# Kernel optimization log

Measured on AMD Instinct MI355X. Metric: run time of the kernel, lower is better.

The kernel has to match this reference:

```python
import jax, jax.numpy as jnp
import numpy as np
from jax import lax

# Model dims (match init_kwargs config)
HID = 2048      # hidden_size
NH = 64         # num_heads
P = 64          # head_dim
N = 128         # ssm_state_size
G = 1           # n_groups
CS = 256        # chunk_size
K = 4           # conv kernel
D_INNER = NH * P                  # 4096
CONV_DIM = D_INNER + 2 * G * N    # 4352
PROJ = D_INNER + CONV_DIM + NH    # 8512
EPS = 1e-5
BATCH, SEQ = 2, 2048


def setup_inputs() -> dict:
    key = jax.random.key(0)
    ks = jax.random.split(key, 8)
    hidden_states = jax.random.normal(ks[0], (BATCH, SEQ, HID), dtype=jnp.float32)
    W_in = jax.random.normal(ks[1], (PROJ, HID), dtype=jnp.float32) * 0.02
    conv_w = jax.random.normal(ks[2], (CONV_DIM, 1, K), dtype=jnp.float32) * 0.2
    conv_b = jax.random.normal(ks[3], (CONV_DIM,), dtype=jnp.float32) * 0.02
    # dt_bias initialized like inv-softplus of dt in [1e-3, 1e-1]
    dt = jnp.exp(jax.random.uniform(ks[4], (NH,)) * (np.log(0.1) - np.log(0.001)) + np.log(0.001))
    dt_bias = (dt + jnp.log(-jnp.expm1(-dt))).astype(jnp.float32)
    A_log = jnp.log(jnp.arange(1, NH + 1, dtype=jnp.float32))
    D_param = jnp.ones((NH,), dtype=jnp.float32)
    norm_w = jnp.ones((D_INNER,), dtype=jnp.float32)
    W_out = jax.random.normal(ks[5], (HID, D_INNER), dtype=jnp.float32) * 0.02
    return {"hidden_states": hidden_states, "W_in": W_in, "conv_w": conv_w,
            "conv_b": conv_b, "dt_bias": dt_bias, "A_log": A_log,
            "D_param": D_param, "norm_w": norm_w, "W_out": W_out}


def _segsum(x):
    # x: (..., c) -> (..., c, c); seg[i, j] = sum_{j < k <= i} x_k (diag 0), -inf above diag
    T = x.shape[-1]
    xc = jnp.cumsum(x, axis=-1)
    seg = xc[..., :, None] - xc[..., None, :]
    mask = jnp.tril(jnp.ones((T, T), dtype=bool))
    return jnp.where(mask, seg, -jnp.inf)


def _mamba2_forward(hidden_states, W_in, conv_w, conv_b, dt_bias, A_log, D_param, norm_w, W_out):
    B_, L_ = hidden_states.shape[:2]
    proj = hidden_states @ W_in.T                           # (b, l, PROJ)
    z = proj[..., :D_INNER]                                 # gate
    xBC = proj[..., D_INNER:D_INNER + CONV_DIM]
    dt = proj[..., D_INNER + CONV_DIM:]                     # (b, l, NH)

    # depthwise causal conv1d + silu
    xc = lax.conv_general_dilated(
        jnp.transpose(xBC, (0, 2, 1)), conv_w,
        window_strides=(1,), padding=[(K - 1, 0)],
        feature_group_count=CONV_DIM)                        # (b, CONV_DIM, l)
    xc = xc + conv_b[None, :, None]
    xBC = jax.nn.silu(jnp.transpose(xc, (0, 2, 1)))          # (b, l, CONV_DIM)

    x = xBC[..., :D_INNER].reshape(B_, L_, NH, P)
    Bm = xBC[..., D_INNER:D_INNER + G * N].reshape(B_, L_, G, N)
    Cm = xBC[..., D_INNER + G * N:].reshape(B_, L_, G, N)

    dt = jax.nn.softplus(dt + dt_bias)                       # (b, l, NH)
    A = -jnp.exp(A_log)                                      # (NH,)

    Bh = jnp.repeat(Bm, NH // G, axis=2)                     # (b, l, h, n)
    Ch = jnp.repeat(Cm, NH // G, axis=2)

    # ---- chunked SSD scan ----
    nc = L_ // CS
    x_dt = (x * dt[..., None]).reshape(B_, nc, CS, NH, P)    # (b, c, s, h, p)
    B_c = Bh.reshape(B_, nc, CS, NH, N)
    C_c = Ch.reshape(B_, nc, CS, NH, N)
    dA = jnp.transpose((dt * A).reshape(B_, nc, CS, NH), (0, 3, 1, 2))  # (b, h, c, s)
    A_cum = jnp.cumsum(dA, axis=-1)                          # (b, h, c, s)

    Lmat = jnp.exp(_segsum(dA))                              # (b, h, c, s, s)
    Y_diag = jnp.einsum('bclhn,bcshn,bhcls,bcshp->bclhp', C_c, B_c, Lmat, x_dt)

    decay_states = jnp.exp(A_cum[..., -1:] - A_cum)          # (b, h, c, s)
    states = jnp.einsum('bclhn,bhcl,bclhp->bchpn', B_c, decay_states, x_dt)

    da_last = A_cum[..., -1]                                 # (b, h, c)

    def step(prev, inp):
        s_k, d_k = inp                                       # (b,h,p,n), (b,h)
        new = prev * jnp.exp(d_k)[..., None, None] + s_k
        return new, prev

    _, prev_states = lax.scan(step, jnp.zeros((B_, NH, P, N), dtype=x.dtype),
                              (jnp.transpose(states, (1, 0, 2, 3, 4)),
                               jnp.transpose(da_last, (2, 0, 1))))
    prev_states = jnp.transpose(prev_states, (1, 2, 0, 3, 4))  # (b, h, c, p, n)

    Y_off = jnp.einsum('bclhn,bhcpn,bhcl->bclhp', C_c, prev_states, jnp.exp(A_cum))

    y = (Y_diag + Y_off).reshape(B_, L_, NH, P) + D_param[None, None, :, None] * x
    y = y.reshape(B_, L_, D_INNER)

    # gated grouped RMSNorm (norm_before_gate=False): norm(y * silu(z)) * w
    g = y * jax.nn.silu(z)
    gs = D_INNER // G
    gr = g.reshape(B_, L_, G, gs)
    var = jnp.mean(gr * gr, axis=-1, keepdims=True)
    gn = (gr * lax.rsqrt(var + EPS)).reshape(B_, L_, D_INNER) * norm_w

    return gn @ W_out.T                                      # (b, l, HID)


def reference(hidden_states, W_in, conv_w, conv_b, dt_bias, A_log, D_param, norm_w, W_out):
    return _mamba2_forward(hidden_states, W_in, conv_w, conv_b, dt_bias, A_log, D_param, norm_w, W_out)
```

## Files before the change

kernel.cpp:

```cpp
#include <hip/hip_runtime.h>

#define SEQLEN 2048
#define NHEADS 64
#define PDIM 64
#define NSTATE 128
#define CSIZE 256
#define NCHUNK 8
#define DINNER 4096
#define CONVD 4352
#define PROJD 8512

using s8v = __attribute__((ext_vector_type(8))) short;
using f4v = __attribute__((ext_vector_type(4))) float;
using bf8v = __attribute__((ext_vector_type(8))) __bf16;

__device__ __forceinline__ short f2bf(float x) {
  union { float f; unsigned u; } t; t.f = x;
  unsigned r = t.u + 0x7FFFu + ((t.u >> 16) & 1u);
  return (short)(r >> 16);
}
__device__ __forceinline__ float bf2f(short s) {
  union { unsigned u; float f; } t;
  t.u = ((unsigned)(unsigned short)s) << 16;
  return t.f;
}

__device__ __forceinline__ f4v mfma_bf16(s8v a, s8v b, f4v c) {
  return __builtin_amdgcn_mfma_f32_16x16x32_bf16(
      __builtin_bit_cast(bf8v, a), __builtin_bit_cast(bf8v, b), c, 0, 0, 0);
}

__device__ __forceinline__ void gll16(const void* g, void* l) {
  __builtin_amdgcn_global_load_lds(
      (const __attribute__((address_space(1))) unsigned*)g,
      (__attribute__((address_space(3))) unsigned*)l, 16, 0, 0);
}

__global__ __launch_bounds__(256) void cast_bf16_kernel(
    const float* __restrict__ in, short* __restrict__ out, int n4) {
  int i = blockIdx.x * 256 + threadIdx.x;
  if (i < n4) {
    float4 v = ((const float4*)in)[i];
    short4 o;
    o.x = f2bf(v.x); o.y = f2bf(v.y); o.z = f2bf(v.z); o.w = f2bf(v.w);
    ((short4*)out)[i] = o;
  }
}


#define G1_STAGE_A(dst, h, kt) do {                                          \
    _Pragma("unroll")                                                        \
    for (int it_ = 0; it_ < 2; ++it_) {                                      \
      int ci_ = it_ * 512 + tid;                                             \
      int r_ = ci_ >> 3;                                                     \
      int g_ = ((ci_ & 7) ^ (r_ & 7)) << 3;                                  \
      gll16(&A[(size_t)(tm0 + (h) * 128 + r_) * 2048 + (kt) * 64 + g_],      \
            &(dst)[(h) * 8192 + ci_ * 8]);                                   \
    }                                                                        \
  } while (0)

#define G1_STAGE_B(dst, h, kt) do {                                          \
    _Pragma("unroll")                                                        \
    for (int it_ = 0; it_ < 2; ++it_) {                                      \
      int ci_ = it_ * 512 + tid;                                             \
      int r_ = ci_ >> 3;                                                     \
      int g_ = ((ci_ & 7) ^ (r_ & 7)) << 3;                                  \
      int br_ = tn0 + (h) * 128 + r_;                                        \
      if (br_ > 8511) br_ = 8511;       \
      gll16(&B[(size_t)br_ * 2048 + (kt) * 64 + g_],                         \
            &(dst)[(h) * 8192 + ci_ * 8]);                                   \
    }                                                                        \
  } while (0)

#define RD_A(m, ks) \
  (*(const s8v*)&Ad[(wm + (m) * 16 + lr) * 64 + (((ks) * 4 + q) ^ sw7) * 8])
#define RD_B(n, ks) \
  (*(const s8v*)&Bd[(wn + (n) * 16 + lr) * 64 + (((ks) * 4 + q) ^ sw7) * 8])

#define G1_PHASE(m0, STAGE_STMT) do {                                        \
    s8v a00 = RD_A(m0, 0), a01 = RD_A(m0, 1);                                \
    s8v a10 = RD_A((m0) + 1, 0), a11 = RD_A((m0) + 1, 1);                    \
    STAGE_STMT;                                                              \
    __builtin_amdgcn_s_barrier();                                            \
    asm volatile("s_waitcnt lgkmcnt(0)" ::: "memory");                       \
    __builtin_amdgcn_s_setprio(1);                                           \
    _Pragma("unroll") for (int n = 0; n < 4; ++n)                            \
      acc[m0][n] = mfma_bf16(a00, bk0[n], acc[m0][n]);                       \
    _Pragma("unroll") for (int n = 0; n < 4; ++n)                            \
      acc[m0][n] = mfma_bf16(a01, bk1[n], acc[m0][n]);                       \
    _Pragma("unroll") for (int n = 0; n < 4; ++n)                            \
      acc[(m0) + 1][n] = mfma_bf16(a10, bk0[n], acc[(m0) + 1][n]);           \
    _Pragma("unroll") for (int n = 0; n < 4; ++n)                            \
      acc[(m0) + 1][n] = mfma_bf16(a11, bk1[n], acc[(m0) + 1][n]);           \
    __builtin_amdgcn_s_setprio(0);                                           \
    __builtin_amdgcn_s_barrier();                                            \
  } while (0)

__global__ __launch_bounds__(512, 2) void gemm1_256(
    const short* __restrict__ A, const short* __restrict__ B,
    short* __restrict__ z, short* __restrict__ xbc, float* __restrict__ dtb) {
  const int NT = 32;
  const int bid = blockIdx.x;
  const int sid = (bid & 7) * 68 + (bid >> 3);
  const int panel = sid / 136, rem = sid % 136;
  const int bx = rem >> 2, by = panel * 4 + (rem & 3);
  const int tm0 = by * 256, tn0 = bx * 256;
  __shared__ alignas(16) short lds[65536];
  const int tid = threadIdx.x;
  const int lane = tid & 63, wid = tid >> 6;
  const int wm = (wid >> 2) * 128, wn = (wid & 3) * 64;
  const int lr = lane & 15, q = lane >> 4;
  const int sw7 = lr & 7;

  f4v acc[8][4];
#pragma unroll
  for (int m = 0; m < 8; ++m)
#pragma unroll
    for (int n = 0; n < 4; ++n)
#pragma unroll
      for (int r = 0; r < 4; ++r) acc[m][n][r] = 0.f;

  {
    short* A0 = lds;
    short* B0 = lds + 16384;
    short* B1 = lds + 49152;
    G1_STAGE_A(A0, 0, 0); G1_STAGE_A(A0, 1, 0);
    G1_STAGE_B(B0, 0, 0); G1_STAGE_B(B0, 1, 0);
    G1_STAGE_B(B1, 0, 1); G1_STAGE_B(B1, 1, 1);
  }

  for (int t = 0; t < NT; ++t) {
    short* Ad = lds + ((t & 1) << 15);
    short* Bd = Ad + 16384;
    short* An = lds + (((t + 1) & 1) << 15);
    s8v bk0[4], bk1[4];
    if (t + 1 < NT) {
      G1_STAGE_A(An, 0, t + 1);
      asm volatile("s_waitcnt vmcnt(6)" ::: "memory");
    } else {
      asm volatile("s_waitcnt vmcnt(0)" ::: "memory");
    }
    __builtin_amdgcn_s_barrier();
#pragma unroll
    for (int n = 0; n < 4; ++n) { bk0[n] = RD_B(n, 0); bk1[n] = RD_B(n, 1); }
    {
      s8v a00 = RD_A(0, 0), a01 = RD_A(0, 1);
      s8v a10 = RD_A(1, 0), a11 = RD_A(1, 1);
      __builtin_amdgcn_s_setprio(1);
#pragma unroll
      for (int n = 0; n < 4; ++n) acc[0][n] = mfma_bf16(a00, bk0[n], acc[0][n]);
#pragma unroll
      for (int n = 0; n < 4; ++n) acc[0][n] = mfma_bf16(a01, bk1[n], acc[0][n]);
#pragma unroll
      for (int n = 0; n < 4; ++n) acc[1][n] = mfma_bf16(a10, bk0[n], acc[1][n]);
#pragma unroll
      for (int n = 0; n < 4; ++n) acc[1][n] = mfma_bf16(a11, bk1[n], acc[1][n]);
      __builtin_amdgcn_s_setprio(0);
    }
    __builtin_amdgcn_s_barrier();
    G1_PHASE(2, if (t + 1 < NT) G1_STAGE_A(An, 1, t + 1));
    G1_PHASE(4, if (t + 2 < NT) G1_STAGE_B(Bd, 0, t + 2));
    G1_PHASE(6, if (t + 2 < NT) G1_STAGE_B(Bd, 1, t + 2));
  }

  if (bx == 33) {
    if (wn == 0) {
#pragma unroll
      for (int m = 0; m < 8; ++m)
#pragma unroll
        for (int n = 0; n < 4; ++n) {
          int col = n * 16 + lr;
#pragma unroll
          for (int r = 0; r < 4; ++r) {
            int row = tm0 + wm + m * 16 + q * 4 + r;
            dtb[(size_t)row * NHEADS + col] = acc[m][n][r];
          }
        }
    }
    return;
  }
  short* outp; int stride, colbase;
  if (bx < 16) { outp = z;   stride = DINNER; colbase = tn0; }
  else         { outp = xbc; stride = CONVD;  colbase = tn0 - DINNER; }
  short* Cs = lds;
  for (int h = 0; h < 2; ++h) {
    __syncthreads();
    if ((wid >> 2) == h) {
#pragma unroll
      for (int m = 0; m < 8; ++m)
#pragma unroll
        for (int n = 0; n < 4; ++n)
#pragma unroll
          for (int r = 0; r < 4; ++r)
            Cs[(m * 16 + q * 4 + r) * 264 + wn + n * 16 + lr] =
                f2bf(acc[m][n][r]);
    }
    __syncthreads();
#pragma unroll
    for (int itr = 0; itr < 8; ++itr) {
      int idx = itr * 512 + tid;
      int r = idx >> 5, c8 = (idx & 31) * 8;
      s8v v = *(const s8v*)&Cs[r * 264 + c8];
      *(s8v*)&outp[(size_t)(tm0 + h * 128 + r) * stride + colbase + c8] = v;
    }
  }
}

__global__ __launch_bounds__(256, 4) void gemm_nt_bf16(
    const short* __restrict__ A, const short* __restrict__ B,
    float* __restrict__ C, int M, int N, int K) {
  const int nbx = N >> 7;
  const int bid0 = blockIdx.x;
  const int bid = (bid0 & 7) * (gridDim.x >> 3) + (bid0 >> 3);
  const int panel = bid / (nbx * 4), rem = bid % (nbx * 4);
  const int bx = rem >> 2, by = panel * 4 + (rem & 3);
  const int tn0 = bx * 128, tm0 = by * 128;
  __shared__ alignas(16) short As[128 * 32];
  __shared__ alignas(16) short Bs[128 * 32];
  const int tid = threadIdx.x;
  const int lane = tid & 63, wid = tid >> 6;
  const int wm = (wid >> 1) * 64, wn = (wid & 1) * 64;
  const int lr = lane & 15, q = lane >> 4;
  const int fA = (lr & 3) ^ ((lr >> 2) & 3);
  const int qs = (q ^ fA) * 8;
  f4v acc[4][4];
  for (int i = 0; i < 4; i++)
    for (int j = 0; j < 4; j++)
      for (int r = 0; r < 4; r++) acc[i][j][r] = 0.f;

  for (int k0 = 0; k0 < K; k0 += 32) {
    __syncthreads();
    for (int it = 0; it < 2; it++) {
      int ci = it * 256 + tid;
      int row = ci >> 2;
      int cg = ((ci & 3) ^ (row & 3) ^ ((row >> 2) & 3)) << 3;
      gll16(&A[(size_t)(tm0 + row) * K + k0 + cg], &As[ci * 8]);
      gll16(&B[(size_t)(tn0 + row) * K + k0 + cg], &Bs[ci * 8]);
    }
    __syncthreads();
    s8v af[4], bfr[4];
    for (int i = 0; i < 4; i++) af[i]  = *(const s8v*)&As[(wm + i * 16 + lr) * 32 + qs];
    for (int j = 0; j < 4; j++) bfr[j] = *(const s8v*)&Bs[(wn + j * 16 + lr) * 32 + qs];
    for (int i = 0; i < 4; i++)
      for (int j = 0; j < 4; j++)
        acc[i][j] = mfma_bf16(af[i], bfr[j], acc[i][j]);
  }
  for (int i = 0; i < 4; i++)
    for (int j = 0; j < 4; j++) {
      int r0 = tm0 + wm + i * 16 + q * 4;
      int c0 = tn0 + wn + j * 16 + lr;
      for (int r = 0; r < 4; r++)
        C[(size_t)(r0 + r) * N + c0] = acc[i][j][r];
    }
}

__global__ __launch_bounds__(256) void conv_silu_kernel(
    const short* __restrict__ xbc, const float* __restrict__ conv_w,
    const float* __restrict__ conv_b, short* __restrict__ xBCc) {
  int cc = blockIdx.x * 256 + threadIdx.x;
  int bl = blockIdx.y;
  int b = bl >> 11, l = bl & 2047;
  float4 wv = *(const float4*)&conv_w[cc * 4];
  float wk[4] = {wv.x, wv.y, wv.z, wv.w};
  float acc = conv_b[cc];
  const short* pbase = xbc + (size_t)(b * SEQLEN) * CONVD + cc;
#pragma unroll
  for (int k = 0; k < 4; k++) {
    int ls = l - 3 + k;
    if (ls >= 0) acc += bf2f(pbase[(size_t)ls * CONVD]) * wk[k];
  }
  float sv = acc / (1.f + expf(-acc));
  xBCc[(size_t)bl * CONVD + cc] = f2bf(sv);
}

__global__ __launch_bounds__(256) void dt_kernel(
    float* __restrict__ dtb, const float* __restrict__ dt_bias) {
  int idx = blockIdx.x * 256 + threadIdx.x;
  int hh = idx & 63;
  float v = dtb[idx] + dt_bias[hh];
  dtb[idx] = (v > 20.f) ? v : log1pf(expf(v));
}

__global__ __launch_bounds__(256) void ssd_states_kernel(
    const short* __restrict__ xBCc, const float* __restrict__ dtp,
    const float* __restrict__ A_log, short* __restrict__ states,
    float* __restrict__ da_last) {
  const int blk = blockIdx.x;
  const int h = blk & 63, cc = (blk >> 6) & 7, b = blk >> 9;
  const int tid = threadIdx.x;
  __shared__ float dt_s[CSIZE], Acum[CSIZE], w_s[CSIZE];
  __shared__ float xw[64][64];
  __shared__ float Bt[64][NSTATE];
  const size_t row0 = (size_t)(b * SEQLEN + cc * CSIZE);
  dt_s[tid] = dtp[(row0 + tid) * NHEADS + h];
  __syncthreads();
  if (tid == 0) {
    float Aval = -expf(A_log[h]);
    float s = 0.f;
    for (int i = 0; i < CSIZE; i++) { s += dt_s[i]; Acum[i] = s * Aval; }
    da_last[(size_t)(b * NHEADS + h) * NCHUNK + cc] = Acum[CSIZE - 1];
  }
  __syncthreads();
  float total = Acum[CSIZE - 1];
  w_s[tid] = dt_s[tid] * expf(total - Acum[tid]);
  float acc[4][8];
  for (int a = 0; a < 4; a++) for (int j = 0; j < 8; j++) acc[a][j] = 0.f;
  const int pi = (tid & 15) * 4, ni = (tid >> 4) * 8;
  for (int lt = 0; lt < 4; lt++) {
    __syncthreads();
    for (int i = 0; i < 4; i++) {
      int idx = tid + i * 256;
      int r = idx >> 4, c4 = (idx & 15) << 2;
      short4 v = *(const short4*)&xBCc[(row0 + lt * 64 + r) * CONVD + h * PDIM + c4];
      float wl = w_s[lt * 64 + r];
      xw[r][c4 + 0] = bf2f(v.x) * wl;
      xw[r][c4 + 1] = bf2f(v.y) * wl;
      xw[r][c4 + 2] = bf2f(v.z) * wl;
      xw[r][c4 + 3] = bf2f(v.w) * wl;
    }
    for (int i = 0; i < 8; i++) {
      int idx = tid + i * 256;
      int r = idx >> 5, c4 = (idx & 31) << 2;
      short4 v = *(const short4*)&xBCc[(row0 + lt * 64 + r) * CONVD + DINNER + c4];
      Bt[r][c4 + 0] = bf2f(v.x);
      Bt[r][c4 + 1] = bf2f(v.y);
      Bt[r][c4 + 2] = bf2f(v.z);
      Bt[r][c4 + 3] = bf2f(v.w);
    }
    __syncthreads();
    for (int l = 0; l < 64; l++) {
      float4 xv = *(const float4*)&xw[l][pi];
      float4 b0 = *(const float4*)&Bt[l][ni];
      float4 b1 = *(const float4*)&Bt[l][ni + 4];
      float xa[4] = {xv.x, xv.y, xv.z, xv.w};
      float bb[8] = {b0.x, b0.y, b0.z, b0.w, b1.x, b1.y, b1.z, b1.w};
      for (int a = 0; a < 4; a++)
        for (int j = 0; j < 8; j++)
          acc[a][j] += xa[a] * bb[j];
    }
  }
  const size_t sbase = (((size_t)b * NCHUNK + cc) * NHEADS + h) * (PDIM * NSTATE);
  for (int a = 0; a < 4; a++) {
    short o[8];
    for (int j = 0; j < 8; j++) o[j] = f2bf(acc[a][j]);
    *(s8v*)&states[sbase + (size_t)(pi + a) * NSTATE + ni] = *(const s8v*)o;
  }
}

__global__ __launch_bounds__(256) void scan_kernel(
    short* __restrict__ states, const float* __restrict__ da_last) {
  const int bh = blockIdx.x >> 2, sl = blockIdx.x & 3;
  const int b = bh >> 6, h = bh & 63;
  const int tid = threadIdx.x;
  float prev[8];
  for (int i = 0; i < 8; i++) prev[i] = 0.f;
  for (int c = 0; c < NCHUNK; c++) {
    const size_t base = (((size_t)b * NCHUNK + c) * NHEADS + h) * (PDIM * NSTATE)
                      + sl * 2048;
    const float d = expf(da_last[(size_t)bh * NCHUNK + c]);
    for (int i = 0; i < 8; i++) {
      size_t e = base + tid + i * 256;
      float s = bf2f(states[e]);
      states[e] = f2bf(prev[i]);
      prev[i] = prev[i] * d + s;
    }
  }
}

__global__ __launch_bounds__(256) void ssd_y_kernel(
    const short* __restrict__ xBCc, const float* __restrict__ dtp,
    const float* __restrict__ A_log, const float* __restrict__ D_param,
    const short* __restrict__ prevs, short* __restrict__ y) {
  const int blk = blockIdx.x;
  const int h = blk & 63, cc = (blk >> 6) & 7, b = blk >> 9;
  const int tid = threadIdx.x;
  const int lane = tid & 63, w = tid >> 6;
  const int lr = lane & 15, q = lane >> 4;
  __shared__ float dt_s[CSIZE];
  __shared__ float Acum[CSIZE];
  __shared__ short C_s[64][136];
  __shared__ short BP_s[64][136];
  __shared__ short xdtT[64][72];
  __shared__ short Mt[64][72];
  const size_t row0 = (size_t)(b * SEQLEN + cc * CSIZE);
  dt_s[tid] = dtp[(row0 + tid) * NHEADS + h];
  __syncthreads();
  if (tid == 0) {
    float Aval = -expf(A_log[h]);
    float s = 0.f;
    for (int i = 0; i < CSIZE; i++) { s += dt_s[i]; Acum[i] = s * Aval; }
  }
  const float Dh = D_param[h];
  const size_t prevbase = (((size_t)b * NCHUNK + cc) * NHEADS + h) * (PDIM * NSTATE);
  const int wl0 = w * 16;

  for (int lt = 0; lt < 4; lt++) {
    __syncthreads();
    for (int i = 0; i < 4; i++) {
      int idx = tid + i * 256;
      int r = idx >> 4, c8 = (idx & 15) << 3;
      *(s8v*)&C_s[r][c8] =
          *(const s8v*)&xBCc[(row0 + lt * 64 + r) * CONVD + DINNER + NSTATE + c8];
      *(s8v*)&BP_s[r][c8] = *(const s8v*)&prevs[prevbase + (size_t)r * NSTATE + c8];
    }
    __syncthreads();
    f4v acc[4];
    for (int j = 0; j < 4; j++) for (int r = 0; r < 4; r++) acc[j][r] = 0.f;
    for (int ks = 0; ks < 4; ks++) {
      s8v a = *(const s8v*)&C_s[wl0 + lr][ks * 32 + q * 8];
      for (int j = 0; j < 4; j++) {
        s8v bb = *(const s8v*)&BP_s[j * 16 + lr][ks * 32 + q * 8];
        acc[j] = mfma_bf16(a, bb, acc[j]);
      }
    }
    for (int r = 0; r < 4; r++) {
      float e = __expf(Acum[lt * 64 + wl0 + q * 4 + r]);
      for (int j = 0; j < 4; j++) acc[j][r] *= e;
    }
    for (int st = 0; st <= lt; st++) {
      __syncthreads();
      for (int i = 0; i < 4; i++) {
        int idx = tid + i * 256;
        int r = idx >> 4, c8 = (idx & 15) << 3;
        *(s8v*)&BP_s[r][c8] =
            *(const s8v*)&xBCc[(row0 + st * 64 + r) * CONVD + DINNER + c8];
      }
      for (int i = 0; i < 4; i++) {
        int idx = tid + i * 256;
        int r = idx >> 4, c4 = (idx & 15) << 2;
        float dtv = dt_s[st * 64 + r];
        short4 v = *(const short4*)&xBCc[(row0 + st * 64 + r) * CONVD + h * PDIM + c4];
        xdtT[c4 + 0][r] = f2bf(bf2f(v.x) * dtv);
        xdtT[c4 + 1][r] = f2bf(bf2f(v.y) * dtv);
        xdtT[c4 + 2][r] = f2bf(bf2f(v.z) * dtv);
        xdtT[c4 + 3][r] = f2bf(bf2f(v.w) * dtv);
      }
      __syncthreads();
      f4v sacc[4];
      for (int j = 0; j < 4; j++) for (int r = 0; r < 4; r++) sacc[j][r] = 0.f;
      for (int ks = 0; ks < 4; ks++) {
        s8v a = *(const s8v*)&C_s[wl0 + lr][ks * 32 + q * 8];
        for (int j = 0; j < 4; j++) {
          s8v bb = *(const s8v*)&BP_s[j * 16 + lr][ks * 32 + q * 8];
          sacc[j] = mfma_bf16(a, bb, sacc[j]);
        }
      }
      int lbase = lt * 64 + wl0 + q * 4;
      for (int j = 0; j < 4; j++) {
        int sg = st * 64 + j * 16 + lr;
        for (int r = 0; r < 4; r++) {
          int ll = lbase + r;
          float m = (sg <= ll) ? sacc[j][r] * __expf(Acum[ll] - Acum[sg]) : 0.f;
          Mt[wl0 + q * 4 + r][j * 16 + lr] = f2bf(m);
        }
      }
      __syncthreads();
      for (int ss2 = 0; ss2 < 2; ss2++) {
        s8v a = *(const s8v*)&Mt[wl0 + lr][ss2 * 32 + q * 8];
        for (int j = 0; j < 4; j++) {
          s8v bb = *(const s8v*)&xdtT[j * 16 + lr][ss2 * 32 + q * 8];
          acc[j] = mfma_bf16(a, bb, acc[j]);
        }
      }
    }
    for (int j = 0; j < 4; j++)
      for (int r = 0; r < 4; r++) {
        int lrow = wl0 + q * 4 + r;
        int ll = lt * 64 + lrow;
        int p = j * 16 + lr;
        float xv = bf2f(xBCc[(row0 + ll) * CONVD + h * PDIM + p]);
        Mt[lrow][p] = f2bf(acc[j][r] + Dh * xv);
      }
    __syncthreads();
    for (int ps = 0; ps < 2; ps++) {
      int r = ps * 32 + (tid >> 3);
      int c8 = (tid & 7) * 8;
      s8v v = *(const s8v*)&Mt[r][c8];
      *(s8v*)&y[(row0 + lt * 64 + r) * DINNER + h * PDIM + c8] = v;
    }
  }
}

__global__ __launch_bounds__(256) void norm_kernel(
    const short* __restrict__ y, const short* __restrict__ z,
    const float* __restrict__ norm_w, short* __restrict__ g) {
  int bl = blockIdx.x, tid = threadIdx.x;
  const short4* yrow = (const short4*)(y + (size_t)bl * DINNER);
  const short4* zrow = (const short4*)(z + (size_t)bl * DINNER);
  float gv[16];
  float ss = 0.f;
  for (int i = 0; i < 4; i++) {
    short4 yv = yrow[tid + i * 256];
    short4 zv = zrow[tid + i * 256];
    float zf[4] = {bf2f(zv.x), bf2f(zv.y), bf2f(zv.z), bf2f(zv.w)};
    float yf[4] = {bf2f(yv.x), bf2f(yv.y), bf2f(yv.z), bf2f(yv.w)};
    for (int t = 0; t < 4; t++) {
      float gg = yf[t] * (zf[t] / (1.f + expf(-zf[t])));
      gv[i * 4 + t] = gg;
      ss += gg * gg;
    }
  }
  for (int off = 32; off > 0; off >>= 1) ss += __shfl_down(ss, off);
  __shared__ float red[4];
  __shared__ float rsS;
  if ((tid & 63) == 0) red[tid >> 6] = ss;
  __syncthreads();
  if (tid == 0) rsS = rsqrtf((red[0] + red[1] + red[2] + red[3]) * (1.f / 4096.f) + 1e-5f);
  __syncthreads();
  float rs = rsS;
  for (int i = 0; i < 4; i++) {
    int j4 = (tid + i * 256) * 4;
    float4 nw = *(const float4*)&norm_w[j4];
    short4 o;
    o.x = f2bf(gv[i * 4 + 0] * rs * nw.x);
    o.y = f2bf(gv[i * 4 + 1] * rs * nw.y);
    o.z = f2bf(gv[i * 4 + 2] * rs * nw.z);
    o.w = f2bf(gv[i * 4 + 3] * rs * nw.w);
    *(short4*)&g[(size_t)bl * DINNER + j4] = o;
  }
}

extern "C" void kernel_launch(void* const* d_in, const int* in_sizes, int n_in,
                              void* d_out, int out_size, void* d_ws, size_t ws_size,
                              hipStream_t stream) {
  const float* hidden  = (const float*)d_in[0];
  const float* W_in    = (const float*)d_in[1];
  const float* conv_w  = (const float*)d_in[2];
  const float* conv_b  = (const float*)d_in[3];
  const float* dt_bias = (const float*)d_in[4];
  const float* A_log   = (const float*)d_in[5];
  const float* D_param = (const float*)d_in[6];
  const float* norm_w  = (const float*)d_in[7];
  const float* W_out   = (const float*)d_in[8];
  float* out = (float*)d_out;

  char* ws = (char*)d_ws;
  short* z_bf  = (short*)(ws + 0);
  float* dtb   = (float*)(ws + 33554432);
  float* da_l  = (float*)(ws + 34603008);
  short* xbc_pre = (short*)(ws + 34607104);
  short* y_bf    = (short*)(ws + 34607104);
  short* hid_bf  = (short*)(ws + 70258688);
  short* win_bf  = (short*)(ws + 87035904);
  short* xBCc    = (short*)(ws + 70258688);
  short* states  = (short*)(ws + 105910272);
  short* g_bf    = (short*)(ws + 70258688);
  short* wout_bf = (short*)(ws + 105910272);
  if (ws_size < (size_t)122687488) return;

  cast_bf16_kernel<<<8192, 256, 0, stream>>>(hidden, hid_bf, 2097152);
  cast_bf16_kernel<<<17024, 256, 0, stream>>>(W_in, win_bf, 4358144);

  gemm1_256<<<544, 512, 0, stream>>>(hid_bf, win_bf, z_bf, xbc_pre, dtb);

  conv_silu_kernel<<<dim3(17, 4096), 256, 0, stream>>>(xbc_pre, conv_w, conv_b, xBCc);
  dt_kernel<<<1024, 256, 0, stream>>>(dtb, dt_bias);

  ssd_states_kernel<<<1024, 256, 0, stream>>>(xBCc, dtb, A_log, states, da_l);
  scan_kernel<<<512, 256, 0, stream>>>(states, da_l);
  ssd_y_kernel<<<1024, 256, 0, stream>>>(xBCc, dtb, A_log, D_param, states, y_bf);

  norm_kernel<<<4096, 256, 0, stream>>>(y_bf, z_bf, norm_w, g_bf);
  cast_bf16_kernel<<<8192, 256, 0, stream>>>(W_out, wout_bf, 2097152);

  gemm_nt_bf16<<<512, 256, 0, stream>>>(g_bf, wout_bf, out, 4096, 2048, 4096);
}
```

Baseline: 665.1 us.

## Restructure gemm1 pipeline into four uniform phases with end-of-iteration vmcnt wait

Reorganizes the main loop of the input-projection GEMM so that every K-tile iteration runs four identical phases. Each phase issues its LDS reads and the next global-to-LDS stage, then does a barrier and runs its MFMAs. The global-load wait moves from the start of each iteration to the last phase of the previous one, and a wait-plus-barrier is added after the prologue. The goal is to remove the separate top-of-iteration barrier and the vmcnt stall before the first MFMAs, so loads overlap more with compute. Getting the vmcnt counts or the buffer reuse wrong could cause stale-data races.

```diff
diff --git a/kernel.cpp b/kernel.cpp
--- a/kernel.cpp
+++ b/kernel.cpp
@@ -77,23 +77,17 @@
 #define RD_B(n, ks) \
   (*(const s8v*)&Bd[(wn + (n) * 16 + lr) * 64 + (((ks) * 4 + q) ^ sw7) * 8])
 
-#define G1_PHASE(m0, STAGE_STMT) do {                                        \
-    s8v a00 = RD_A(m0, 0), a01 = RD_A(m0, 1);                                \
-    s8v a10 = RD_A((m0) + 1, 0), a11 = RD_A((m0) + 1, 1);                    \
-    STAGE_STMT;                                                              \
-    __builtin_amdgcn_s_barrier();                                            \
-    asm volatile("s_waitcnt lgkmcnt(0)" ::: "memory");                       \
+#define G1_MFMA2(m0, x00, x01, x10, x11) do {                                \
     __builtin_amdgcn_s_setprio(1);                                           \
     _Pragma("unroll") for (int n = 0; n < 4; ++n)                            \
-      acc[m0][n] = mfma_bf16(a00, bk0[n], acc[m0][n]);                       \
+      acc[m0][n] = mfma_bf16(x00, bk0[n], acc[m0][n]);                       \
     _Pragma("unroll") for (int n = 0; n < 4; ++n)                            \
-      acc[m0][n] = mfma_bf16(a01, bk1[n], acc[m0][n]);                       \
+      acc[m0][n] = mfma_bf16(x01, bk1[n], acc[m0][n]);                       \
     _Pragma("unroll") for (int n = 0; n < 4; ++n)                            \
-      acc[(m0) + 1][n] = mfma_bf16(a10, bk0[n], acc[(m0) + 1][n]);           \
+      acc[(m0) + 1][n] = mfma_bf16(x10, bk0[n], acc[(m0) + 1][n]);           \
     _Pragma("unroll") for (int n = 0; n < 4; ++n)                            \
-      acc[(m0) + 1][n] = mfma_bf16(a11, bk1[n], acc[(m0) + 1][n]);           \
+      acc[(m0) + 1][n] = mfma_bf16(x11, bk1[n], acc[(m0) + 1][n]);           \
     __builtin_amdgcn_s_setprio(0);                                           \
-    __builtin_amdgcn_s_barrier();                                            \
   } while (0)
 
 __global__ __launch_bounds__(512, 2) void gemm1_256(
@@ -127,6 +121,8 @@
     G1_STAGE_A(A0, 0, 0); G1_STAGE_A(A0, 1, 0);
     G1_STAGE_B(B0, 0, 0); G1_STAGE_B(B0, 1, 0);
     G1_STAGE_B(B1, 0, 1); G1_STAGE_B(B1, 1, 1);
+    asm volatile("s_waitcnt vmcnt(4)" ::: "memory");
+    __builtin_amdgcn_s_barrier();
   }
 
   for (int t = 0; t < NT; ++t) {
@@ -134,33 +130,49 @@
     short* Bd = Ad + 16384;
     short* An = lds + (((t + 1) & 1) << 15);
     s8v bk0[4], bk1[4];
-    if (t + 1 < NT) {
-      G1_STAGE_A(An, 0, t + 1);
-      asm volatile("s_waitcnt vmcnt(6)" ::: "memory");
-    } else {
-      asm volatile("s_waitcnt vmcnt(0)" ::: "memory");
-    }
-    __builtin_amdgcn_s_barrier();
-#pragma unroll
-    for (int n = 0; n < 4; ++n) { bk0[n] = RD_B(n, 0); bk1[n] = RD_B(n, 1); }
     {
+#pragma unroll
+      for (int n = 0; n < 4; ++n) { bk0[n] = RD_B(n, 0); bk1[n] = RD_B(n, 1); }
       s8v a00 = RD_A(0, 0), a01 = RD_A(0, 1);
       s8v a10 = RD_A(1, 0), a11 = RD_A(1, 1);
-      __builtin_amdgcn_s_setprio(1);
-#pragma unroll
-      for (int n = 0; n < 4; ++n) acc[0][n] = mfma_bf16(a00, bk0[n], acc[0][n]);
-#pragma unroll
-      for (int n = 0; n < 4; ++n) acc[0][n] = mfma_bf16(a01, bk1[n], acc[0][n]);
-#pragma unroll
-      for (int n = 0; n < 4; ++n) acc[1][n] = mfma_bf16(a10, bk0[n], acc[1][n]);
-#pragma unroll
-      for (int n = 0; n < 4; ++n) acc[1][n] = mfma_bf16(a11, bk1[n], acc[1][n]);
-      __builtin_amdgcn_s_setprio(0);
-    }
-    __builtin_amdgcn_s_barrier();
-    G1_PHASE(2, if (t + 1 < NT) G1_STAGE_A(An, 1, t + 1));
-    G1_PHASE(4, if (t + 2 < NT) G1_STAGE_B(Bd, 0, t + 2));
-    G1_PHASE(6, if (t + 2 < NT) G1_STAGE_B(Bd, 1, t + 2));
+      if (t + 1 < NT) G1_STAGE_A(An, 0, t + 1);
+      __builtin_amdgcn_s_barrier();
+      asm volatile("s_waitcnt lgkmcnt(0)" ::: "memory");
+      G1_MFMA2(0, a00, a01, a10, a11);
+      __builtin_amdgcn_s_barrier();
+    }
+    {
+      s8v a00 = RD_A(2, 0), a01 = RD_A(2, 1);
+      s8v a10 = RD_A(3, 0), a11 = RD_A(3, 1);
+      if (t + 1 < NT) G1_STAGE_A(An, 1, t + 1);
+      __builtin_amdgcn_s_barrier();
+      asm volatile("s_waitcnt lgkmcnt(0)" ::: "memory");
+      G1_MFMA2(2, a00, a01, a10, a11);
+      __builtin_amdgcn_s_barrier();
+    }
+    {
+      s8v a00 = RD_A(4, 0), a01 = RD_A(4, 1);
+      s8v a10 = RD_A(5, 0), a11 = RD_A(5, 1);
+      if (t + 2 < NT) G1_STAGE_B(Bd, 0, t + 2);
+      __builtin_amdgcn_s_barrier();
+      asm volatile("s_waitcnt lgkmcnt(0)" ::: "memory");
+      G1_MFMA2(4, a00, a01, a10, a11);
+      __builtin_amdgcn_s_barrier();
+    }
+    {
+      s8v a00 = RD_A(6, 0), a01 = RD_A(6, 1);
+      s8v a10 = RD_A(7, 0), a11 = RD_A(7, 1);
+      if (t + 2 < NT) G1_STAGE_B(Bd, 1, t + 2);
+      if (t < NT - 2) {
+        asm volatile("s_waitcnt vmcnt(4)" ::: "memory");
+      } else {
+        asm volatile("s_waitcnt vmcnt(0)" ::: "memory");
+      }
+      __builtin_amdgcn_s_barrier();
+      asm volatile("s_waitcnt lgkmcnt(0)" ::: "memory");
+      G1_MFMA2(6, a00, a01, a10, a11);
+      __builtin_amdgcn_s_barrier();
+    }
   }
 
   if (bx == 33) {
```

Result: no change. 673.5 us (+1.3%).
